# Kernel optimization log

Measured on AMD Instinct MI355X. Metric: run time of the kernel, lower is better.

## Reference

```python
import jax, jax.numpy as jnp
import numpy as np

B, L, D, E = 16, 1024, 512, 8
DFF = 4 * D
N_VIEWS, N_BUCKETS = 4, 16


def setup_inputs() -> dict:
    key = jax.random.key(0)
    ks = jax.random.split(key, 9)
    s_in = 1.0 / np.sqrt(D)
    s_hid = 1.0 / np.sqrt(DFF)
    return {
        "x": jax.random.normal(ks[0], (B, L, D), dtype=jnp.float32),
        "view_ids": jax.random.randint(ks[1], (B,), 0, N_VIEWS),
        "visit_ids": jax.random.randint(ks[2], (B,), 0, N_BUCKETS),
        "router_view": jax.random.normal(ks[3], (N_VIEWS, E), dtype=jnp.float32),
        "router_visit": jax.random.normal(ks[4], (N_BUCKETS, E), dtype=jnp.float32),
        "W1": jax.random.uniform(ks[5], (E, D, DFF), jnp.float32, -s_in, s_in),
        "b1": jax.random.uniform(ks[6], (E, DFF), jnp.float32, -s_in, s_in),
        "W2": jax.random.uniform(ks[7], (E, DFF, D), jnp.float32, -s_hid, s_hid),
        "b2": jax.random.uniform(ks[8], (E, D), jnp.float32, -s_hid, s_hid),
    }


def reference(x, view_ids, visit_ids, router_view, router_visit, W1, b1, W2, b2):
    # Router: per-sample logits over experts, (B, E)
    logits = router_view[view_ids] + router_visit[visit_ids]
    top1 = jnp.argmax(logits, axis=-1)  # (B,)

    # Train-mode balance loss: load = mean softmax prob per expert, entropy-style term
    probs = jax.nn.softmax(logits, axis=-1)
    load = probs.mean(axis=0)  # (E,)
    balance_loss = -jnp.sum(load * jnp.log(load))

    # Per-sample expert FFN: gather each sample's expert weights (dense grouped GEMM
    # equivalent of the original masked gather->FFN->scatter loop).
    w1 = W1[top1]                      # (B, D, DFF)
    w2 = W2[top1]                      # (B, DFF, D)
    h = jax.nn.relu(jnp.einsum("bld,bdf->blf", x, w1) + b1[top1][:, None, :])
    out = jnp.einsum("blf,bfd->bld", h, w2) + b2[top1][:, None, :]
    return out, balance_loss
```

## Files before the change

kernel.cpp:

```cpp
#include <hip/hip_runtime.h>
#include <stdint.h>

#define B_SZ 16
#define L_SZ 1024
#define D_SZ 512
#define E_SZ 8
#define DFF_SZ 2048

typedef short bf16x8 __attribute__((ext_vector_type(8)));
typedef float f32x4 __attribute__((ext_vector_type(4)));

__device__ __forceinline__ unsigned short f2bf(float f) {
  unsigned int u = __float_as_uint(f);
  u += 0x7fffu + ((u >> 16) & 1u);
  return (unsigned short)(u >> 16);
}

__device__ __forceinline__ void async_cp16(void* lds, const void* g) {
  __builtin_amdgcn_global_load_lds(
      (const __attribute__((address_space(1))) void*)g,
      (__attribute__((address_space(3))) void*)lds, 16, 0, 0);
}

__device__ __forceinline__ void transpose_body(const float* __restrict__ src,
                                               unsigned short* __restrict__ dst,
                                               int K, int N, int bx, int by,
                                               int bz, float (*tile)[65]) {
  const int n0 = bx * 64;
  const int k0 = by * 64;
  const int t = threadIdx.x;
  {
    const int c4 = (t & 15) * 4;
    const int r = t >> 4;
    const float* s = src + ((size_t)bz * K + k0) * N + n0;
#pragma unroll
    for (int i = 0; i < 4; ++i) {
      const int k = r + i * 16;
      const float4 v = *(const float4*)(s + (size_t)k * N + c4);
      tile[k][c4] = v.x; tile[k][c4 + 1] = v.y;
      tile[k][c4 + 2] = v.z; tile[k][c4 + 3] = v.w;
    }
  }
  __syncthreads();
  {
    const int k4 = (t & 15) * 4;
    const int r = t >> 4;
    unsigned short* d = dst + ((size_t)bz * N + n0) * K + k0;
#pragma unroll
    for (int i = 0; i < 4; ++i) {
      const int n = r + i * 16;
      ushort4 o;
      o.x = f2bf(tile[k4 + 0][n]); o.y = f2bf(tile[k4 + 1][n]);
      o.z = f2bf(tile[k4 + 2][n]); o.w = f2bf(tile[k4 + 3][n]);
      *(ushort4*)(d + (size_t)n * K + k4) = o;
    }
  }
}

__global__ __launch_bounds__(256) void prep_kernel(
    const float* __restrict__ x, unsigned short* __restrict__ xb,
    const float* __restrict__ W1, unsigned short* __restrict__ w1t,
    const float* __restrict__ W2, unsigned short* __restrict__ w2t,
    const int* __restrict__ view_ids, const int* __restrict__ visit_ids,
    const float* __restrict__ rview, const float* __restrict__ rvisit,
    int* __restrict__ top1, float* __restrict__ loss_out) {
  __shared__ float tile[64][65];
  __shared__ float probs[B_SZ][E_SZ];
  const int b = blockIdx.x;
  if (b < 8192) {
    const int i = b * 256 + threadIdx.x;
    const float4 v = reinterpret_cast<const float4*>(x)[i];
    ushort4 o;
    o.x = f2bf(v.x); o.y = f2bf(v.y); o.z = f2bf(v.z); o.w = f2bf(v.w);
    reinterpret_cast<ushort4*>(xb)[i] = o;
  } else if (b < 10240) {
    const int i = b - 8192;
    transpose_body(W1, w1t, D_SZ, DFF_SZ, i & 31, (i >> 5) & 7, i >> 8, tile);
  } else if (b < 12288) {
    const int i = b - 10240;
    transpose_body(W2, w2t, DFF_SZ, D_SZ, i & 7, (i >> 3) & 31, i >> 8, tile);
  } else {
    const int t = threadIdx.x;
    if (t < B_SZ) {
      const int vi = view_ids[t];
      const int si = visit_ids[t];
      float lg[E_SZ];
#pragma unroll
      for (int e = 0; e < E_SZ; ++e)
        lg[e] = rview[vi * E_SZ + e] + rvisit[si * E_SZ + e];
      int am = 0;
      float bm = lg[0];
#pragma unroll
      for (int e = 1; e < E_SZ; ++e)
        if (lg[e] > bm) { bm = lg[e]; am = e; }
      top1[t] = am;
      float s = 0.f;
#pragma unroll
      for (int e = 0; e < E_SZ; ++e) {
        const float p = expf(lg[e] - bm);
        probs[t][e] = p;
        s += p;
      }
      const float inv = 1.f / s;
#pragma unroll
      for (int e = 0; e < E_SZ; ++e) probs[t][e] *= inv;
    }
    __syncthreads();
    if (t == 0) {
      float loss = 0.f;
#pragma unroll
      for (int e = 0; e < E_SZ; ++e) {
        float ld = 0.f;
        for (int bb = 0; bb < B_SZ; ++bb) ld += probs[bb][e];
        ld *= (1.0f / B_SZ);
        loss -= ld * logf(ld);
      }
      *loss_out = loss;
    }
  }
}

template <int BN, int WN2, int NTILES, bool RELU, bool OUT_BF16>
__global__ __launch_bounds__(512, 2) void gemm8_kernel(
    const unsigned short* __restrict__ A,
    const unsigned short* __restrict__ BT,
    const float* __restrict__ bias,
    const int* __restrict__ top1,
    void* __restrict__ Out,
    int N, int K) {
  constexpr int HB = BN / 2;
  constexpr int WM2 = 8 / WN2;
  constexpr int RPA = 128 / WM2;
  constexpr int RPB = HB / WN2;
  constexpr int MF = RPA / 16;
  constexpr int NF = RPB / 16;
  constexpr int LB = HB / 64;
  constexpr int ABUF = 2 * 128 * 64;
  constexpr int BBUF = 2 * HB * 64;
  constexpr int BUFSZ = ABUF + BBUF;

  __shared__ __align__(16) unsigned short sm[2 * BUFSZ];

  const int t = threadIdx.x;
  const int lane = t & 63;
  const int wid = t >> 6;
  const int wm2 = wid / WN2;
  const int wn2 = wid % WN2;
  const int lr = lane & 15, lg = lane >> 4;

  const int nwg = gridDim.x;
  const int bid = blockIdx.x;
  const int wg = (bid & 7) * (nwg >> 3) + (bid >> 3);
  const int mt = wg / NTILES;
  const int nt = wg % NTILES;
  const int n0 = nt * BN;
  const int bz = mt >> 2;
  const int e = top1[bz];

  const size_t Kb = (size_t)K * 2;
  const int srow = t >> 3;
  const int sgr = (t & 7) ^ (srow & 7);
  const char* aRow = (const char*)A + ((size_t)mt * 256 + srow) * Kb + sgr * 16;
  const char* bRow =
      (const char*)BT + ((size_t)e * N + n0 + srow) * Kb + sgr * 16;

  auto stageA = [&](int buf, int half, int kt) {
    char* dst =
        (char*)sm + (size_t)(buf * BUFSZ + half * (128 * 64)) * 2 + t * 16;
    const char* s = aRow + (size_t)(half * 128) * Kb + (size_t)kt * 128;
    async_cp16(dst, s);
    async_cp16(dst + 8192, s + 64 * Kb);
  };
  auto stageB = [&](int buf, int half, int kt) {
    char* dst = (char*)sm + (size_t)(buf * BUFSZ + ABUF + half * (HB * 64)) * 2 +
                t * 16;
    const char* s = bRow + (size_t)(half * HB) * Kb + (size_t)kt * 128;
    async_cp16(dst, s);
    if constexpr (LB == 2) async_cp16(dst + 8192, s + 64 * Kb);
  };

  f32x4 acc[2][2][MF][NF] = {};
  bf16x8 af[MF][2];
  bf16x8 bg[2][NF][2];
  const int nk = K >> 6;

#define READ_A(HALF)                                                          \
  {                                                                           \
    const char* ap = bufBase + (size_t)(HALF) * (128 * 64 * 2);               \
    _Pragma("unroll") for (int mf = 0; mf < MF; ++mf) {                       \
      const int row = wm2 * RPA + mf * 16 + lr;                               \
      _Pragma("unroll") for (int ks = 0; ks < 2; ++ks)                        \
          af[mf][ks] = *(const bf16x8*)(ap + row * 128 +                      \
                                        (((ks * 4 + lg) ^ (lr & 7)) << 4));   \
    }                                                                         \
  }
#define READ_B(Q, HALF)                                                       \
  {                                                                           \
    const char* bp =                                                          \
        bufBase + (size_t)ABUF * 2 + (size_t)(HALF) * (HB * 64 * 2);          \
    _Pragma("unroll") for (int nf = 0; nf < NF; ++nf) {                       \
      const int row = wn2 * RPB + nf * 16 + lr;                               \
      _Pragma("unroll") for (int ks = 0; ks < 2; ++ks)                        \
          bg[Q][nf][ks] = *(const bf16x8*)(bp + row * 128 +                   \
                                           (((ks * 4 + lg) ^ (lr & 7)) << 4)); \
    }                                                                         \
  }
#define MMA(QM, QN)                                                           \
  __builtin_amdgcn_s_setprio(1);                                              \
  _Pragma("unroll") for (int ks = 0; ks < 2; ++ks)                            \
      _Pragma("unroll") for (int mf = 0; mf < MF; ++mf)                       \
          _Pragma("unroll") for (int nf = 0; nf < NF; ++nf)                   \
              acc[QM][QN][mf][nf] = __builtin_amdgcn_mfma_f32_16x16x32_bf16(  \
                  af[mf][ks], bg[QN][nf][ks], acc[QM][QN][mf][nf], 0, 0, 0);  \
  __builtin_amdgcn_s_setprio(0);
#define BAR                                                                   \
  __builtin_amdgcn_s_barrier();                                               \
  asm volatile("" ::: "memory");

  stageA(0, 0, 0); stageB(0, 0, 0); stageA(0, 1, 0); stageB(0, 1, 0);
  stageA(1, 0, 1); stageB(1, 0, 1);
  if constexpr (LB == 2) asm volatile("s_waitcnt vmcnt(4)" ::: "memory");
  else                   asm volatile("s_waitcnt vmcnt(3)" ::: "memory");
  BAR;

  for (int kt = 0; kt < nk; ++kt) {
    const int bi = kt & 1;
    const char* bufBase = (const char*)sm + (size_t)bi * BUFSZ * 2;
    READ_A(0);
    READ_B(0, 0);
    READ_B(1, 1);
    if (kt + 1 < nk) stageA(bi ^ 1, 1, kt + 1);
    MMA(0, 0);
    if (kt + 1 < nk) stageB(bi ^ 1, 1, kt + 1);
    MMA(0, 1);
    BAR;
    READ_A(1);
    if (kt + 2 < nk) stageA(bi, 0, kt + 2);
    MMA(1, 0);
    if (kt + 2 < nk) stageB(bi, 0, kt + 2);
    MMA(1, 1);
    if (kt + 2 < nk) {
      if constexpr (LB == 2) asm volatile("s_waitcnt vmcnt(4)" ::: "memory");
      else                   asm volatile("s_waitcnt vmcnt(3)" ::: "memory");
    } else {
      asm volatile("s_waitcnt vmcnt(0)" ::: "memory");
    }
    BAR;
  }
#undef READ_A
#undef READ_B
#undef MMA
#undef BAR

  const size_t mrow0 = (size_t)mt * 256;
  const float* bp = bias + (size_t)e * N + n0;
  unsigned short* ho = (unsigned short*)Out;
  float* fo = (float*)Out;
#pragma unroll
  for (int qm = 0; qm < 2; ++qm)
#pragma unroll
    for (int mf = 0; mf < MF; ++mf) {
      const int row0 = qm * 128 + wm2 * RPA + mf * 16 + lg * 4;
#pragma unroll
      for (int qn = 0; qn < 2; ++qn)
#pragma unroll
        for (int nf = 0; nf < NF; ++nf) {
          const int col = qn * HB + wn2 * RPB + nf * 16 + lr;
          const float bv = bp[col];
#pragma unroll
          for (int r = 0; r < 4; ++r) {
            float v = acc[qm][qn][mf][nf][r] + bv;
            if (RELU) v = fmaxf(v, 0.f);
            const size_t o = (mrow0 + row0 + r) * (size_t)N + n0 + col;
            if (OUT_BF16) ho[o] = f2bf(v);
            else fo[o] = v;
          }
        }
    }
}

extern "C" void kernel_launch(void* const* d_in, const int* in_sizes, int n_in,
                              void* d_out, int out_size, void* d_ws,
                              size_t ws_size, hipStream_t stream) {
  const float* x = (const float*)d_in[0];
  const int* view_ids = (const int*)d_in[1];
  const int* visit_ids = (const int*)d_in[2];
  const float* rview = (const float*)d_in[3];
  const float* rvisit = (const float*)d_in[4];
  const float* W1 = (const float*)d_in[5];
  const float* b1 = (const float*)d_in[6];
  const float* W2 = (const float*)d_in[7];
  const float* b2 = (const float*)d_in[8];
  float* out = (float*)d_out;

  char* ws = (char*)d_ws;
  int* top1 = (int*)ws;
  unsigned short* x_bf = (unsigned short*)(ws + 256);
  unsigned short* w1t = (unsigned short*)(ws + 256 + 16777216L);
  unsigned short* w2t = (unsigned short*)(ws + 256 + 2 * 16777216L);
  unsigned short* h_bf = (unsigned short*)(ws + 256 + 3 * 16777216L);

  prep_kernel<<<12289, 256, 0, stream>>>(
      x, x_bf, W1, w1t, W2, w2t, view_ids, visit_ids, rview, rvisit, top1,
      out + (size_t)B_SZ * L_SZ * D_SZ);

  gemm8_kernel<256, 4, 8, true, true><<<512, 512, 0, stream>>>(
      x_bf, w1t, b1, top1, (void*)h_bf, DFF_SZ, D_SZ);
  gemm8_kernel<128, 2, 4, false, false><<<256, 512, 0, stream>>>(
      h_bf, w2t, b2, top1, (void*)out, D_SZ, DFF_SZ);
}
```

Measured before the change: 233.4 us.

## Switch GEMMs to 256x128 tiles with triple-buffered LDS and staged epilogue

Replaces the split-half 8-wave ping-pong GEMM with a single 256x128 tile per workgroup, a three-stage LDS ring that prefetches two k-steps ahead with one barrier per iteration, and a 4x4 MFMA fragment per wave. The epilogue now writes biased, activated results to LDS first and then stores them to global memory as vectorised rows (float4 or packed bf16x4) instead of scattered scalar stores. GEMM1 now launches twice as many blocks because its N tile is narrower. The aim is fewer barriers and coalesced output writes, at the cost of more LDS per block (72KB), which may limit occupancy, and less A-tile reuse in GEMM1.

```diff
diff --git a/kernel.cpp b/kernel.cpp
--- a/kernel.cpp
+++ b/kernel.cpp
@@ -120,32 +120,22 @@
   }
 }
 
-template <int BN, int WN2, int NTILES, bool RELU, bool OUT_BF16>
-__global__ __launch_bounds__(512, 2) void gemm8_kernel(
+template <int NTILES, bool RELU, bool OUT_BF16>
+__global__ __launch_bounds__(512, 2) void gemm_kernel(
     const unsigned short* __restrict__ A,
     const unsigned short* __restrict__ BT,
     const float* __restrict__ bias,
     const int* __restrict__ top1,
     void* __restrict__ Out,
     int N, int K) {
-  constexpr int HB = BN / 2;
-  constexpr int WM2 = 8 / WN2;
-  constexpr int RPA = 128 / WM2;
-  constexpr int RPB = HB / WN2;
-  constexpr int MF = RPA / 16;
-  constexpr int NF = RPB / 16;
-  constexpr int LB = HB / 64;
-  constexpr int ABUF = 2 * 128 * 64;
-  constexpr int BBUF = 2 * HB * 64;
-  constexpr int BUFSZ = ABUF + BBUF;
-
-  __shared__ __align__(16) unsigned short sm[2 * BUFSZ];
+  constexpr int BUFB = (256 + 128) * 64 * 2;
+  __shared__ __align__(16) unsigned short sm[3 * (256 + 128) * 64];
 
   const int t = threadIdx.x;
   const int lane = t & 63;
   const int wid = t >> 6;
-  const int wm2 = wid / WN2;
-  const int wn2 = wid % WN2;
+  const int wm = wid >> 1;
+  const int wn = wid & 1;
   const int lr = lane & 15, lg = lane >> 4;
 
   const int nwg = gridDim.x;
@@ -153,7 +143,7 @@
   const int wg = (bid & 7) * (nwg >> 3) + (bid >> 3);
   const int mt = wg / NTILES;
   const int nt = wg % NTILES;
-  const int n0 = nt * BN;
+  const int n0 = nt * 128;
   const int bz = mt >> 2;
   const int e = top1[bz];
 
@@ -164,119 +154,105 @@
   const char* bRow =
       (const char*)BT + ((size_t)e * N + n0 + srow) * Kb + sgr * 16;
 
-  auto stageA = [&](int buf, int half, int kt) {
-    char* dst =
-        (char*)sm + (size_t)(buf * BUFSZ + half * (128 * 64)) * 2 + t * 16;
-    const char* s = aRow + (size_t)(half * 128) * Kb + (size_t)kt * 128;
-    async_cp16(dst, s);
-    async_cp16(dst + 8192, s + 64 * Kb);
+  auto stage = [&](int buf, int kt) {
+    char* dst = (char*)sm + (size_t)buf * BUFB + t * 16;
+    const char* sa = aRow + (size_t)kt * 128;
+#pragma unroll
+    for (int c = 0; c < 4; ++c)
+      async_cp16(dst + c * 8192, sa + (size_t)c * 64 * Kb);
+    char* dstB = (char*)sm + (size_t)buf * BUFB + 32768 + t * 16;
+    const char* sb = bRow + (size_t)kt * 128;
+#pragma unroll
+    for (int c = 0; c < 2; ++c)
+      async_cp16(dstB + c * 8192, sb + (size_t)c * 64 * Kb);
   };
-  auto stageB = [&](int buf, int half, int kt) {
-    char* dst = (char*)sm + (size_t)(buf * BUFSZ + ABUF + half * (HB * 64)) * 2 +
-                t * 16;
-    const char* s = bRow + (size_t)(half * HB) * Kb + (size_t)kt * 128;
-    async_cp16(dst, s);
-    if constexpr (LB == 2) async_cp16(dst + 8192, s + 64 * Kb);
-  };
-
-  f32x4 acc[2][2][MF][NF] = {};
-  bf16x8 af[MF][2];
-  bf16x8 bg[2][NF][2];
+
+  f32x4 acc[4][4] = {};
+  bf16x8 af[4][2], bg[4][2];
   const int nk = K >> 6;
 
-#define READ_A(HALF)                                                          \
-  {                                                                           \
-    const char* ap = bufBase + (size_t)(HALF) * (128 * 64 * 2);               \
-    _Pragma("unroll") for (int mf = 0; mf < MF; ++mf) {                       \
-      const int row = wm2 * RPA + mf * 16 + lr;                               \
-      _Pragma("unroll") for (int ks = 0; ks < 2; ++ks)                        \
-          af[mf][ks] = *(const bf16x8*)(ap + row * 128 +                      \
-                                        (((ks * 4 + lg) ^ (lr & 7)) << 4));   \
-    }                                                                         \
-  }
-#define READ_B(Q, HALF)                                                       \
-  {                                                                           \
-    const char* bp =                                                          \
-        bufBase + (size_t)ABUF * 2 + (size_t)(HALF) * (HB * 64 * 2);          \
-    _Pragma("unroll") for (int nf = 0; nf < NF; ++nf) {                       \
-      const int row = wn2 * RPB + nf * 16 + lr;                               \
-      _Pragma("unroll") for (int ks = 0; ks < 2; ++ks)                        \
-          bg[Q][nf][ks] = *(const bf16x8*)(bp + row * 128 +                   \
-                                           (((ks * 4 + lg) ^ (lr & 7)) << 4)); \
-    }                                                                         \
-  }
-#define MMA(QM, QN)                                                           \
-  __builtin_amdgcn_s_setprio(1);                                              \
-  _Pragma("unroll") for (int ks = 0; ks < 2; ++ks)                            \
-      _Pragma("unroll") for (int mf = 0; mf < MF; ++mf)                       \
-          _Pragma("unroll") for (int nf = 0; nf < NF; ++nf)                   \
-              acc[QM][QN][mf][nf] = __builtin_amdgcn_mfma_f32_16x16x32_bf16(  \
-                  af[mf][ks], bg[QN][nf][ks], acc[QM][QN][mf][nf], 0, 0, 0);  \
-  __builtin_amdgcn_s_setprio(0);
-#define BAR                                                                   \
-  __builtin_amdgcn_s_barrier();                                               \
+  stage(0, 0);
+  stage(1, 1);
+  asm volatile("s_waitcnt vmcnt(6)" ::: "memory");
+  __builtin_amdgcn_s_barrier();
   asm volatile("" ::: "memory");
 
-  stageA(0, 0, 0); stageB(0, 0, 0); stageA(0, 1, 0); stageB(0, 1, 0);
-  stageA(1, 0, 1); stageB(1, 0, 1);
-  if constexpr (LB == 2) asm volatile("s_waitcnt vmcnt(4)" ::: "memory");
-  else                   asm volatile("s_waitcnt vmcnt(3)" ::: "memory");
-  BAR;
-
+  int cur = 0;
   for (int kt = 0; kt < nk; ++kt) {
-    const int bi = kt & 1;
-    const char* bufBase = (const char*)sm + (size_t)bi * BUFSZ * 2;
-    READ_A(0);
-    READ_B(0, 0);
-    READ_B(1, 1);
-    if (kt + 1 < nk) stageA(bi ^ 1, 1, kt + 1);
-    MMA(0, 0);
-    if (kt + 1 < nk) stageB(bi ^ 1, 1, kt + 1);
-    MMA(0, 1);
-    BAR;
-    READ_A(1);
-    if (kt + 2 < nk) stageA(bi, 0, kt + 2);
-    MMA(1, 0);
-    if (kt + 2 < nk) stageB(bi, 0, kt + 2);
-    MMA(1, 1);
+    const int s2 = cur ? cur - 1 : 2;
+    if (kt + 2 < nk) stage(s2, kt + 2);
+    const char* bufA = (const char*)sm + (size_t)cur * BUFB;
+    const char* bufB = bufA + 32768;
+#pragma unroll
+    for (int mf = 0; mf < 4; ++mf) {
+      const int row = wm * 64 + mf * 16 + lr;
+#pragma unroll
+      for (int ks = 0; ks < 2; ++ks)
+        af[mf][ks] = *(const bf16x8*)(bufA + row * 128 +
+                                      (((ks * 4 + lg) ^ (lr & 7)) << 4));
+    }
+#pragma unroll
+    for (int nf = 0; nf < 4; ++nf) {
+      const int row = wn * 64 + nf * 16 + lr;
+#pragma unroll
+      for (int ks = 0; ks < 2; ++ks)
+        bg[nf][ks] = *(const bf16x8*)(bufB + row * 128 +
+                                      (((ks * 4 + lg) ^ (lr & 7)) << 4));
+    }
+    __builtin_amdgcn_s_setprio(1);
+#pragma unroll
+    for (int ks = 0; ks < 2; ++ks)
+#pragma unroll
+      for (int mf = 0; mf < 4; ++mf)
+#pragma unroll
+        for (int nf = 0; nf < 4; ++nf)
+          acc[mf][nf] = __builtin_amdgcn_mfma_f32_16x16x32_bf16(
+              af[mf][ks], bg[nf][ks], acc[mf][nf], 0, 0, 0);
+    __builtin_amdgcn_s_setprio(0);
     if (kt + 2 < nk) {
-      if constexpr (LB == 2) asm volatile("s_waitcnt vmcnt(4)" ::: "memory");
-      else                   asm volatile("s_waitcnt vmcnt(3)" ::: "memory");
+      asm volatile("s_waitcnt vmcnt(6)" ::: "memory");
     } else {
       asm volatile("s_waitcnt vmcnt(0)" ::: "memory");
     }
-    BAR;
-  }
-#undef READ_A
-#undef READ_B
-#undef MMA
-#undef BAR
-
-  const size_t mrow0 = (size_t)mt * 256;
-  const float* bp = bias + (size_t)e * N + n0;
+    __builtin_amdgcn_s_barrier();
+    asm volatile("" ::: "memory");
+    cur = (cur == 2) ? 0 : cur + 1;
+  }
+
+  float* wb = (float*)sm + (size_t)wid * (64 * 68);
+  const float* bp = bias + (size_t)e * N + n0 + wn * 64;
+  float bv[4];
+#pragma unroll
+  for (int j = 0; j < 4; ++j) bv[j] = bp[j * 16 + lr];
+#pragma unroll
+  for (int i = 0; i < 4; ++i)
+#pragma unroll
+    for (int j = 0; j < 4; ++j)
+#pragma unroll
+      for (int r = 0; r < 4; ++r) {
+        const int row = i * 16 + lg * 4 + r;
+        const int col = j * 16 + lr;
+        float v = acc[i][j][r] + bv[j];
+        if (RELU) v = fmaxf(v, 0.f);
+        wb[row * 68 + col] = v;
+      }
   unsigned short* ho = (unsigned short*)Out;
   float* fo = (float*)Out;
-#pragma unroll
-  for (int qm = 0; qm < 2; ++qm)
-#pragma unroll
-    for (int mf = 0; mf < MF; ++mf) {
-      const int row0 = qm * 128 + wm2 * RPA + mf * 16 + lg * 4;
-#pragma unroll
-      for (int qn = 0; qn < 2; ++qn)
-#pragma unroll
-        for (int nf = 0; nf < NF; ++nf) {
-          const int col = qn * HB + wn2 * RPB + nf * 16 + lr;
-          const float bv = bp[col];
-#pragma unroll
-          for (int r = 0; r < 4; ++r) {
-            float v = acc[qm][qn][mf][nf][r] + bv;
-            if (RELU) v = fmaxf(v, 0.f);
-            const size_t o = (mrow0 + row0 + r) * (size_t)N + n0 + col;
-            if (OUT_BF16) ho[o] = f2bf(v);
-            else fo[o] = v;
-          }
-        }
-    }
+  const size_t gr0 = (size_t)mt * 256 + wm * 64;
+  const int gc0 = n0 + wn * 64 + lr * 4;
+#pragma unroll
+  for (int it = 0; it < 16; ++it) {
+    const int row = it * 4 + lg;
+    const float4 v = *(const float4*)&wb[row * 68 + lr * 4];
+    const size_t o = (gr0 + row) * (size_t)N + gc0;
+    if (OUT_BF16) {
+      ushort4 u;
+      u.x = f2bf(v.x); u.y = f2bf(v.y); u.z = f2bf(v.z); u.w = f2bf(v.w);
+      *(ushort4*)&ho[o] = u;
+    } else {
+      *(float4*)&fo[o] = v;
+    }
+  }
 }
 
 extern "C" void kernel_launch(void* const* d_in, const int* in_sizes, int n_in,
@@ -304,8 +280,8 @@
       x, x_bf, W1, w1t, W2, w2t, view_ids, visit_ids, rview, rvisit, top1,
       out + (size_t)B_SZ * L_SZ * D_SZ);
 
-  gemm8_kernel<256, 4, 8, true, true><<<512, 512, 0, stream>>>(
+  gemm_kernel<16, true, true><<<1024, 512, 0, stream>>>(
       x_bf, w1t, b1, top1, (void*)h_bf, DFF_SZ, D_SZ);
-  gemm8_kernel<128, 2, 4, false, false><<<256, 512, 0, stream>>>(
+  gemm_kernel<4, false, false><<<256, 512, 0, stream>>>(
       h_bf, w2t, b2, top1, (void*)out, D_SZ, DFF_SZ);
 }
```

New measurement: 240.7 us. 3.1% more time.
